# Kernel tuning notes

Hardware: AMD Instinct MI355X
Metric: run time of the kernel (lower is better)

## Reference

```python
import jax, jax.numpy as jnp
import numpy as np

M, IN, OUT, R = 8192, 4096, 4096, 16  # tokens, in_features, out_features, lora rank


def setup_inputs() -> dict:
    key = jax.random.key(0)
    k = jax.random.split(key, 7)
    # symmetric int8 quantized activations and weights
    x = jax.random.randint(k[0], (M, IN), -127, 128, dtype=jnp.int8)
    weight = jax.random.randint(k[1], (OUT, IN), -127, 128, dtype=jnp.int8)
    # per-token activation scales and per-output-channel weight scales
    x_scales = jax.random.uniform(k[2], (M,), jnp.float32, 0.5, 1.5) / 127.0
    scales = jax.random.uniform(k[3], (OUT,), jnp.float32, 0.5, 1.5) / 127.0
    bias = jax.random.normal(k[4], (OUT,), jnp.float32)
    # module inits lora_a ~ N(0, 1/r); lora_b is zeros in the module but we use
    # small random values so the LoRA path is numerically exercised
    lora_a = jax.random.normal(k[5], (R, IN), jnp.float32) * (1.0 / R)
    lora_b = jax.random.normal(k[6], (OUT, R), jnp.float32) * 0.02
    return dict(x=x, weight=weight, bias=bias, x_scales=x_scales,
                scales=scales, lora_a=lora_a, lora_b=lora_b, fuse_gelu=1)


def reference(x, weight, bias, x_scales, scales, lora_a, lora_b, fuse_gelu):
    acc = jax.lax.dot_general(x, weight, (((1,), (1,)), ((), ())),
                              preferred_element_type=jnp.int32)
    # dequantize with outer product of per-token and per-channel scales
    main = acc.astype(jnp.float32) * x_scales[:, None] * scales[None, :]
    # LoRA correction on the dequantized activations: (x_deq @ A^T) @ B^T
    x_deq = x.astype(jnp.float32) * x_scales[:, None]          # [M, IN]
    lora = (x_deq @ lora_a.T) @ lora_b.T                        # [M, R] @ [R, OUT]
    out = main + lora + bias[None, :]
    if fuse_gelu:  # static Python flag
        out = jax.nn.gelu(out, approximate=True)  # tanh-approx GELU (CUDA fused path)
    return out
```

## Files before the change

### kernel.cpp

```cpp
#include <hip/hip_runtime.h>

#define M_DIM 8192
#define IN_DIM 4096
#define OUT_DIM 4096

typedef int   v4i  __attribute__((ext_vector_type(4)));
typedef int   v16i __attribute__((ext_vector_type(16)));
typedef short v8s  __attribute__((ext_vector_type(8)));
typedef float v4f  __attribute__((ext_vector_type(4)));
typedef float v16f __attribute__((ext_vector_type(16)));

static __device__ __forceinline__ int pack4(int a, int b, int c, int d) {
    return (a & 255) | ((b & 255) << 8) | ((c & 255) << 16) | ((d & 255) << 24);
}

static __device__ __forceinline__ short f2bf(float f) {
    unsigned u = __float_as_uint(f);
    u = (u + 0x7FFFu + ((u >> 16) & 1u)) >> 16;
    return (short)u;
}

static __device__ __forceinline__ short i2bf(int v) {
    float f = (float)v;
    return (short)(__float_as_uint(f) >> 16);
}

static __device__ __forceinline__ float gelu_tanh(float u) {
    float u2 = u * u;
    float p  = fmaf(u2, 0.0356774081f, 0.7978845608f);
    float v  = u * p;
    float e  = __builtin_amdgcn_exp2f(v * 2.8853900818f);
    return u - u * __builtin_amdgcn_rcpf(e + 1.0f);
}

static __device__ __forceinline__ void async_cp16(const signed char* g, signed char* l) {
    __builtin_amdgcn_global_load_lds((const __attribute__((address_space(1))) void*)g,
                                     (__attribute__((address_space(3))) void*)l, 16, 0, 0);
}


__global__ __launch_bounds__(256) void pack_a_kernel(const float* __restrict__ la,
                                                     short* __restrict__ a16,
                                                     float* __restrict__ T) {
    const int flat = blockIdx.x * 256 + threadIdx.x;
    size_t i = (size_t)flat * 4;
    float4 a = *(const float4*)(la + i);
    short4 o;
    o.x = f2bf(a.x); o.y = f2bf(a.y); o.z = f2bf(a.z); o.w = f2bf(a.w);
    *(short4*)(a16 + i) = o;
    float4 z = {0.f, 0.f, 0.f, 0.f};
    float4* tz = (float4*)(T + (size_t)flat * 8);
    tz[0] = z; tz[1] = z;
}

static __device__ __forceinline__ void do_pack_w(int flat, const int* __restrict__ w,
                                                 signed char* __restrict__ w8t) {
    const int l  = flat & 63;
    const int gp = (flat >> 6) & 15;
    const int kk = (flat >> 10) & 63;
    const int bn = flat >> 16;
    const int n = bn * 256 + ((gp >> 1) << 5) + (l & 31);
    const int k = kk * 64 + ((gp & 1) << 5) + ((l >> 5) << 4);
    const int4* p = (const int4*)(w + (size_t)n * IN_DIM + k);
    int4 a = p[0], b = p[1], c = p[2], d = p[3];
    int4 o;
    o.x = pack4(a.x, a.y, a.z, a.w);
    o.y = pack4(b.x, b.y, b.z, b.w);
    o.z = pack4(c.x, c.y, c.z, c.w);
    o.w = pack4(d.x, d.y, d.z, d.w);
    *(int4*)(w8t + (size_t)flat * 16) = o;
}

static __device__ __forceinline__ void do_pack_x(int blk, int tid, float* red,
                                                 const int* __restrict__ x,
                                                 const short* __restrict__ a16,
                                                 signed char* __restrict__ x8t,
                                                 float* __restrict__ T) {
    const int lane = tid & 63, wv = tid >> 6;
    const int fr = lane & 15, fq = lane >> 4;
    const int m0 = (blk >> 3) * 16;
    const int ks = blk & 7;
    const int bm = m0 >> 8;
    const int g  = (m0 >> 5) & 7;
    const int l5 = (m0 & 16) + fr;
    const int row = m0 + fr;

    v4f acc = {0.f, 0.f, 0.f, 0.f};
#pragma unroll 4
    for (int kt = 0; kt < 4; ++kt) {
        const int k  = ks * 512 + wv * 128 + kt * 32 + fq * 8;
        const int4* xp = (const int4*)(x + (size_t)row * IN_DIM + k);
        int4 a = xp[0], b = xp[1];
        const int kk = k >> 6, c = (k >> 4) & 3, j8 = (k >> 3) & 1;
        int2 pk = make_int2(pack4(a.x, a.y, a.z, a.w), pack4(b.x, b.y, b.z, b.w));
        *(int2*)(x8t + ((size_t)((bm * 64 + kk) * 16 + g * 2 + (c >> 1))) * 1024 +
                 ((c & 1) * 32 + l5) * 16 + j8 * 8) = pk;
        v8s xa;
        xa[0] = i2bf(a.x); xa[1] = i2bf(a.y); xa[2] = i2bf(a.z); xa[3] = i2bf(a.w);
        xa[4] = i2bf(b.x); xa[5] = i2bf(b.y); xa[6] = i2bf(b.z); xa[7] = i2bf(b.w);
        v8s aa = *(const v8s*)(a16 + (size_t)fr * IN_DIM + k);
        acc = __builtin_amdgcn_mfma_f32_16x16x32_bf16(xa, aa, acc, 0, 0, 0);
    }
    *(v4f*)&red[wv * 256 + lane * 4] = acc;
    __syncthreads();

    float s = red[tid] + red[256 + tid] + red[512 + tid] + red[768 + tid];
    const int sl = tid >> 2, j = tid & 3;
    const int r16 = ((sl >> 4) << 2) + j, col = sl & 15;
    atomicAdd(&T[(size_t)(m0 + r16) * 16 + col], s);
}

__global__ __launch_bounds__(256) void pack_xw_kernel(const int* __restrict__ x,
                                                      const short* __restrict__ a16,
                                                      signed char* __restrict__ x8t,
                                                      float* __restrict__ T,
                                                      const int* __restrict__ w,
                                                      signed char* __restrict__ w8t) {
    __shared__ float red[4 * 256];
    const int b = blockIdx.x;
    if (b < 4096) {
        do_pack_x(b, threadIdx.x, red, x, a16, x8t, T);
    } else {
        do_pack_w((b - 4096) * 256 + threadIdx.x, w, w8t);
    }
}

__global__ __launch_bounds__(256) void pack_w_kernel(const int* __restrict__ w,
                                                     signed char* __restrict__ w8t) {
    do_pack_w(blockIdx.x * 256 + threadIdx.x, w, w8t);
}

__global__ __launch_bounds__(256) void pack_x_lora_kernel(const int* __restrict__ x,
                                                          const short* __restrict__ a16,
                                                          signed char* __restrict__ x8t,
                                                          float* __restrict__ T) {
    __shared__ float red[4 * 256];
    do_pack_x(blockIdx.x, threadIdx.x, red, x, a16, x8t, T);
}

__global__ __launch_bounds__(256, 2) void q8_gemm_kernel(
    const signed char* __restrict__ x8t, const signed char* __restrict__ w8t,
    const float* __restrict__ Tp, const float* __restrict__ lbm,
    const float* __restrict__ bias, const float* __restrict__ xsc,
    const float* __restrict__ wsc, const int* __restrict__ gflag,
    float* __restrict__ out) {
    __shared__ __align__(16) signed char smem[73728];

    const int tid  = threadIdx.x;
    const int lane = tid & 63;
    const int wv   = tid >> 6;
    const int wm   = wv >> 1, wn = wv & 1;
    const int b   = blockIdx.x;
    const int xcd = b & 7, rr = b >> 3;
    const int bm  = xcd * 4 + (rr & 3);
    const int bn  = rr >> 2;

    const int lofs = lane * 16;
    const size_t toff = (size_t)tid * 16;
    const signed char* Asrc = x8t + (size_t)bm * (64 * 16 * 1024);
    const signed char* Bsrc = w8t + (size_t)(bn >> 1) * (64 * 16 * 1024) + (bn & 1) * 8192;

    v16i acc[4][2];
    {
        v16i z;
#pragma unroll
        for (int i = 0; i < 16; ++i) z[i] = 0;
#pragma unroll
        for (int mt = 0; mt < 4; ++mt)
#pragma unroll
            for (int nt = 0; nt < 2; ++nt) acc[mt][nt] = z;
    }

#pragma unroll
    for (int tt = 0; tt < 2; ++tt) {
        const signed char* gA = Asrc + (size_t)tt * 16384 + toff;
        const signed char* gB = Bsrc + (size_t)tt * 16384 + toff;
        signed char* sA = smem + tt * 24576 + (wv << 10);
        signed char* sB = sA + 16384;
        async_cp16(gA,         sA);
        async_cp16(gA + 4096,  sA + 4096);
        async_cp16(gA + 8192,  sA + 8192);
        async_cp16(gA + 12288, sA + 12288);
        async_cp16(gB,         sB);
        async_cp16(gB + 4096,  sB + 4096);
    }
    asm volatile("s_waitcnt vmcnt(6)" ::: "memory");
    __builtin_amdgcn_s_barrier();

    int cur = 0;
    for (int t = 0; t < 64; ++t) {
        const signed char* Ab = smem + cur * 24576;
        const signed char* Bb = Ab + 16384;
        const int sb = (cur == 0) ? 2 : cur - 1;
        signed char* sA = smem + sb * 24576 + (wv << 10);
        signed char* sB = sA + 16384;
        const signed char* gA = Asrc + (size_t)(t + 2) * 16384 + toff;
        const signed char* gB = Bsrc + (size_t)(t + 2) * 16384 + toff;
        const bool pf = (t < 62);

        v4i a0, a1, a2, a3, b0, b1;

        a0 = *(const v4i*)(Ab + ((wm * 4 + 0) * 2 + 0) * 1024 + lofs);
        a1 = *(const v4i*)(Ab + ((wm * 4 + 1) * 2 + 0) * 1024 + lofs);
        a2 = *(const v4i*)(Ab + ((wm * 4 + 2) * 2 + 0) * 1024 + lofs);
        a3 = *(const v4i*)(Ab + ((wm * 4 + 3) * 2 + 0) * 1024 + lofs);
        b0 = *(const v4i*)(Bb + ((wn * 2 + 0) * 2 + 0) * 1024 + lofs);
        b1 = *(const v4i*)(Bb + ((wn * 2 + 1) * 2 + 0) * 1024 + lofs);
        if (pf) {
            async_cp16(gA,        sA);
            async_cp16(gA + 4096, sA + 4096);
            async_cp16(gB,        sB);
        }
        __builtin_amdgcn_s_barrier();
        __builtin_amdgcn_s_setprio(1);
        acc[0][0] = __builtin_amdgcn_mfma_i32_32x32x32_i8(a0, b0, acc[0][0], 0, 0, 0);
        acc[0][1] = __builtin_amdgcn_mfma_i32_32x32x32_i8(a0, b1, acc[0][1], 0, 0, 0);
        acc[1][0] = __builtin_amdgcn_mfma_i32_32x32x32_i8(a1, b0, acc[1][0], 0, 0, 0);
        acc[1][1] = __builtin_amdgcn_mfma_i32_32x32x32_i8(a1, b1, acc[1][1], 0, 0, 0);
        acc[2][0] = __builtin_amdgcn_mfma_i32_32x32x32_i8(a2, b0, acc[2][0], 0, 0, 0);
        acc[2][1] = __builtin_amdgcn_mfma_i32_32x32x32_i8(a2, b1, acc[2][1], 0, 0, 0);
        acc[3][0] = __builtin_amdgcn_mfma_i32_32x32x32_i8(a3, b0, acc[3][0], 0, 0, 0);
        acc[3][1] = __builtin_amdgcn_mfma_i32_32x32x32_i8(a3, b1, acc[3][1], 0, 0, 0);
        __builtin_amdgcn_s_setprio(0);

        a0 = *(const v4i*)(Ab + ((wm * 4 + 0) * 2 + 1) * 1024 + lofs);
        a1 = *(const v4i*)(Ab + ((wm * 4 + 1) * 2 + 1) * 1024 + lofs);
        a2 = *(const v4i*)(Ab + ((wm * 4 + 2) * 2 + 1) * 1024 + lofs);
        a3 = *(const v4i*)(Ab + ((wm * 4 + 3) * 2 + 1) * 1024 + lofs);
        b0 = *(const v4i*)(Bb + ((wn * 2 + 0) * 2 + 1) * 1024 + lofs);
        b1 = *(const v4i*)(Bb + ((wn * 2 + 1) * 2 + 1) * 1024 + lofs);
        if (pf) {
            async_cp16(gA + 8192,  sA + 8192);
            async_cp16(gA + 12288, sA + 12288);
            async_cp16(gB + 4096,  sB + 4096);
        }
        __builtin_amdgcn_s_barrier();
        __builtin_amdgcn_s_setprio(1);
        acc[0][0] = __builtin_amdgcn_mfma_i32_32x32x32_i8(a0, b0, acc[0][0], 0, 0, 0);
        acc[0][1] = __builtin_amdgcn_mfma_i32_32x32x32_i8(a0, b1, acc[0][1], 0, 0, 0);
        acc[1][0] = __builtin_amdgcn_mfma_i32_32x32x32_i8(a1, b0, acc[1][0], 0, 0, 0);
        acc[1][1] = __builtin_amdgcn_mfma_i32_32x32x32_i8(a1, b1, acc[1][1], 0, 0, 0);
        acc[2][0] = __builtin_amdgcn_mfma_i32_32x32x32_i8(a2, b0, acc[2][0], 0, 0, 0);
        acc[2][1] = __builtin_amdgcn_mfma_i32_32x32x32_i8(a2, b1, acc[2][1], 0, 0, 0);
        acc[3][0] = __builtin_amdgcn_mfma_i32_32x32x32_i8(a3, b0, acc[3][0], 0, 0, 0);
        acc[3][1] = __builtin_amdgcn_mfma_i32_32x32x32_i8(a3, b1, acc[3][1], 0, 0, 0);
        __builtin_amdgcn_s_setprio(0);

        if (pf) {
            asm volatile("s_waitcnt vmcnt(6)" ::: "memory");
        } else if (t == 62) {
            asm volatile("s_waitcnt vmcnt(0)" ::: "memory");
        }
        if (t < 63) __builtin_amdgcn_s_barrier();
        cur = (cur == 2) ? 0 : cur + 1;
    }

    const int mbase = bm * 256 + wm * 128;
    const int nbase = bn * 128 + wn * 64;
    const int l31 = lane & 31, lh = lane >> 5;
    const bool dg = (*gflag) != 0;

    v8s tf[4], bf[2];
#pragma unroll
    for (int mt = 0; mt < 4; ++mt) {
        const float* t0 = Tp + (size_t)(mbase + mt * 32 + l31) * 16 + lh * 8;
        v8s v;
#pragma unroll
        for (int j = 0; j < 8; ++j) v[j] = f2bf(t0[j]);
        tf[mt] = v;
    }
#pragma unroll
    for (int nt = 0; nt < 2; ++nt) {
        const float* bp = lbm + (size_t)(nbase + nt * 32 + l31) * 16 + lh * 8;
        v8s v;
#pragma unroll
        for (int j = 0; j < 8; ++j) v[j] = f2bf(bp[j]);
        bf[nt] = v;
    }
    float wsa[2], bba[2];
#pragma unroll
    for (int nt = 0; nt < 2; ++nt) {
        const int col = nbase + nt * 32 + l31;
        wsa[nt] = wsc[col];
        bba[nt] = bias[col];
    }

#pragma unroll
    for (int mt = 0; mt < 4; ++mt) {
        const int rowb = mbase + mt * 32 + lh * 4;
        float4 xs0 = *(const float4*)(xsc + rowb);
        float4 xs1 = *(const float4*)(xsc + rowb + 8);
        float4 xs2 = *(const float4*)(xsc + rowb + 16);
        float4 xs3 = *(const float4*)(xsc + rowb + 24);
        float xsv[16] = {xs0.x, xs0.y, xs0.z, xs0.w, xs1.x, xs1.y, xs1.z, xs1.w,
                         xs2.x, xs2.y, xs2.z, xs2.w, xs3.x, xs3.y, xs3.z, xs3.w};
#pragma unroll
        for (int nt = 0; nt < 2; ++nt) {
            v16f fa;
#pragma unroll
            for (int i = 0; i < 16; ++i) fa[i] = (float)acc[mt][nt][i] * wsa[nt];
            fa = __builtin_amdgcn_mfma_f32_32x32x16_bf16(tf[mt], bf[nt], fa, 0, 0, 0);
            const int col = nbase + nt * 32 + l31;
#pragma unroll
            for (int r = 0; r < 16; ++r) {
                float u = fmaf(xsv[r], fa[r], bba[nt]);
                if (dg) u = gelu_tanh(u);
                out[(size_t)(rowb + (r & 3) + 8 * (r >> 2)) * OUT_DIM + col] = u;
            }
        }
    }
}

extern "C" void kernel_launch(void* const* d_in, const int* in_sizes, int n_in,
                              void* d_out, int out_size, void* d_ws, size_t ws_size,
                              hipStream_t stream) {
    const int*   x     = (const int*)d_in[0];
    const int*   wt    = (const int*)d_in[1];
    const float* bias  = (const float*)d_in[2];
    const float* xsc   = (const float*)d_in[3];
    const float* wsc   = (const float*)d_in[4];
    const float* la    = (const float*)d_in[5];
    const float* lb    = (const float*)d_in[6];
    const int*   gflag = (const int*)d_in[7];
    float* out = (float*)d_out;

    signed char* x8t = (signed char*)d_ws;
    signed char* w8t = x8t + (size_t)M_DIM * IN_DIM;
    float* T = (float*)(w8t + (size_t)OUT_DIM * IN_DIM);

    const size_t base = (size_t)M_DIM * IN_DIM + (size_t)OUT_DIM * IN_DIM +
                        (size_t)M_DIM * 16 * 4;
    const size_t a16_bytes = (size_t)16 * IN_DIM * 2;

    if (ws_size >= base + a16_bytes) {
        short* a16 = (short*)((char*)d_ws + base);
        pack_a_kernel<<<64, 256, 0, stream>>>(la, a16, T);
        pack_xw_kernel<<<8192, 256, 0, stream>>>(x, a16, x8t, T, wt, w8t);
    } else {
        short* a16 = (short*)w8t;
        pack_a_kernel<<<64, 256, 0, stream>>>(la, a16, T);
        pack_x_lora_kernel<<<(M_DIM / 16) * 8, 256, 0, stream>>>(x, a16, x8t, T);
        pack_w_kernel<<<(size_t)OUT_DIM * IN_DIM / (16 * 256), 256, 0, stream>>>(wt, w8t);
    }
    q8_gemm_kernel<<<(M_DIM / 256) * (OUT_DIM / 128), 256, 0, stream>>>(
        x8t, w8t, T, lb, bias, xsc, wsc, gflag, out);
}
```

Measured before the change: 414.2 us.

## Load A fragments directly from global memory and stage only B in LDS

The activation (A) operand no longer goes through the LDS ring buffer. Each wave reads its pre-packed A fragments straight from global memory every k-step, while B stays triple-buffered in LDS, which shrinks shared memory from 72KB to 24KB and cuts the async copies per step. The aim is lower LDS footprint and traffic and fewer copy instructions. In exchange, global-load latency now sits directly in front of the MFMAs with no prefetch. The two waves that share an A tile each fetch it separately, and the compiler's waits on those loads may also drain the outstanding B prefetches.

```diff
diff --git a/kernel.cpp b/kernel.cpp
--- a/kernel.cpp
+++ b/kernel.cpp
@@ -144,7 +144,7 @@
     const float* __restrict__ bias, const float* __restrict__ xsc,
     const float* __restrict__ wsc, const int* __restrict__ gflag,
     float* __restrict__ out) {
-    __shared__ __align__(16) signed char smem[73728];
+    __shared__ __align__(16) signed char smem[24576];
 
     const int tid  = threadIdx.x;
     const int lane = tid & 63;
@@ -173,44 +173,32 @@
 
 #pragma unroll
     for (int tt = 0; tt < 2; ++tt) {
-        const signed char* gA = Asrc + (size_t)tt * 16384 + toff;
         const signed char* gB = Bsrc + (size_t)tt * 16384 + toff;
-        signed char* sA = smem + tt * 24576 + (wv << 10);
-        signed char* sB = sA + 16384;
-        async_cp16(gA,         sA);
-        async_cp16(gA + 4096,  sA + 4096);
-        async_cp16(gA + 8192,  sA + 8192);
-        async_cp16(gA + 12288, sA + 12288);
-        async_cp16(gB,         sB);
-        async_cp16(gB + 4096,  sB + 4096);
-    }
-    asm volatile("s_waitcnt vmcnt(6)" ::: "memory");
+        signed char* sB = smem + tt * 8192 + (wv << 10);
+        async_cp16(gB,        sB);
+        async_cp16(gB + 4096, sB + 4096);
+    }
+    asm volatile("s_waitcnt vmcnt(2)" ::: "memory");
     __builtin_amdgcn_s_barrier();
 
     int cur = 0;
     for (int t = 0; t < 64; ++t) {
-        const signed char* Ab = smem + cur * 24576;
-        const signed char* Bb = Ab + 16384;
+        const signed char* Bb = smem + cur * 8192;
         const int sb = (cur == 0) ? 2 : cur - 1;
-        signed char* sA = smem + sb * 24576 + (wv << 10);
-        signed char* sB = sA + 16384;
-        const signed char* gA = Asrc + (size_t)(t + 2) * 16384 + toff;
+        signed char* sB = smem + sb * 8192 + (wv << 10);
         const signed char* gB = Bsrc + (size_t)(t + 2) * 16384 + toff;
+        const signed char* Ag = Asrc + (size_t)t * 16384;
         const bool pf = (t < 62);
 
         v4i a0, a1, a2, a3, b0, b1;
 
-        a0 = *(const v4i*)(Ab + ((wm * 4 + 0) * 2 + 0) * 1024 + lofs);
-        a1 = *(const v4i*)(Ab + ((wm * 4 + 1) * 2 + 0) * 1024 + lofs);
-        a2 = *(const v4i*)(Ab + ((wm * 4 + 2) * 2 + 0) * 1024 + lofs);
-        a3 = *(const v4i*)(Ab + ((wm * 4 + 3) * 2 + 0) * 1024 + lofs);
+        a0 = *(const v4i*)(Ag + ((wm * 4 + 0) * 2 + 0) * 1024 + lofs);
+        a1 = *(const v4i*)(Ag + ((wm * 4 + 1) * 2 + 0) * 1024 + lofs);
+        a2 = *(const v4i*)(Ag + ((wm * 4 + 2) * 2 + 0) * 1024 + lofs);
+        a3 = *(const v4i*)(Ag + ((wm * 4 + 3) * 2 + 0) * 1024 + lofs);
         b0 = *(const v4i*)(Bb + ((wn * 2 + 0) * 2 + 0) * 1024 + lofs);
         b1 = *(const v4i*)(Bb + ((wn * 2 + 1) * 2 + 0) * 1024 + lofs);
-        if (pf) {
-            async_cp16(gA,        sA);
-            async_cp16(gA + 4096, sA + 4096);
-            async_cp16(gB,        sB);
-        }
+        if (pf) async_cp16(gB, sB);
         __builtin_amdgcn_s_barrier();
         __builtin_amdgcn_s_setprio(1);
         acc[0][0] = __builtin_amdgcn_mfma_i32_32x32x32_i8(a0, b0, acc[0][0], 0, 0, 0);
@@ -223,17 +211,13 @@
         acc[3][1] = __builtin_amdgcn_mfma_i32_32x32x32_i8(a3, b1, acc[3][1], 0, 0, 0);
         __builtin_amdgcn_s_setprio(0);
 
-        a0 = *(const v4i*)(Ab + ((wm * 4 + 0) * 2 + 1) * 1024 + lofs);
-        a1 = *(const v4i*)(Ab + ((wm * 4 + 1) * 2 + 1) * 1024 + lofs);
-        a2 = *(const v4i*)(Ab + ((wm * 4 + 2) * 2 + 1) * 1024 + lofs);
-        a3 = *(const v4i*)(Ab + ((wm * 4 + 3) * 2 + 1) * 1024 + lofs);
+        a0 = *(const v4i*)(Ag + ((wm * 4 + 0) * 2 + 1) * 1024 + lofs);
+        a1 = *(const v4i*)(Ag + ((wm * 4 + 1) * 2 + 1) * 1024 + lofs);
+        a2 = *(const v4i*)(Ag + ((wm * 4 + 2) * 2 + 1) * 1024 + lofs);
+        a3 = *(const v4i*)(Ag + ((wm * 4 + 3) * 2 + 1) * 1024 + lofs);
         b0 = *(const v4i*)(Bb + ((wn * 2 + 0) * 2 + 1) * 1024 + lofs);
         b1 = *(const v4i*)(Bb + ((wn * 2 + 1) * 2 + 1) * 1024 + lofs);
-        if (pf) {
-            async_cp16(gA + 8192,  sA + 8192);
-            async_cp16(gA + 12288, sA + 12288);
-            async_cp16(gB + 4096,  sB + 4096);
-        }
+        if (pf) async_cp16(gB + 4096, sB + 4096);
         __builtin_amdgcn_s_barrier();
         __builtin_amdgcn_s_setprio(1);
         acc[0][0] = __builtin_amdgcn_mfma_i32_32x32x32_i8(a0, b0, acc[0][0], 0, 0, 0);
@@ -247,7 +231,7 @@
         __builtin_amdgcn_s_setprio(0);
 
         if (pf) {
-            asm volatile("s_waitcnt vmcnt(6)" ::: "memory");
+            asm volatile("s_waitcnt vmcnt(2)" ::: "memory");
         } else if (t == 62) {
             asm volatile("s_waitcnt vmcnt(0)" ::: "memory");
         }
```

Result: slower. 456.8 us (+10.3%).
